# Optimization experiments

Measured on AMD Instinct MI355X. Metric: run time of the kernel, lower is better.

## Reference

```python
import jax, jax.numpy as jnp
import numpy as np
from jax import lax

SPATIAL = 4
PAD = 1
STRIDE = 1


def _route(x, rconv_w, rconv_b, fc_w, fc_b, num_experts):
    # x: (b, c, h, w); adaptive avg pool to (SPATIAL, SPATIAL) -- h,w divisible by SPATIAL
    b, c, h, w = x.shape
    pooled = x.reshape(b, c, SPATIAL, h // SPATIAL, SPATIAL, w // SPATIAL).mean(axis=(3, 5))
    # 1x1 conv: (b,c,s,s) x (rc,c) -> (b,rc,s,s)
    y = jnp.einsum('bcij,rc->brij', pooled, rconv_w) + rconv_b[None, :, None, None]
    y = jax.nn.relu(y).reshape(b, -1)                      # (b, rc*s*s)
    y = jax.nn.relu(y @ fc_w.T + fc_b)                     # (b, num_experts*c)
    y = y.reshape(b, num_experts, c)
    return jax.nn.sigmoid(y)                               # (b, k, c)


def _conv_per_sample(xi, wi):
    # xi: (c_in, h, w), wi: (c_out, c_in, kh, kw)
    out = lax.conv_general_dilated(
        xi[None], wi, window_strides=(STRIDE, STRIDE),
        padding=[(PAD, PAD), (PAD, PAD)],
        dimension_numbers=('NCHW', 'OIHW', 'NCHW'))
    return out[0]


def setup_inputs() -> dict:
    key = jax.random.key(0)
    ks = jax.random.split(key, 6)
    b, c_in, c_out, kk, ne = 16, 256, 256, 3, 3
    rc = max(c_in // 16, 16)  # reduction_channels = 16
    x = jax.random.normal(ks[0], (b, c_in, 64, 64), dtype=jnp.float32)
    expert_weight = jax.random.normal(ks[1], (ne, c_out, c_in, kk, kk), dtype=jnp.float32) * 0.02
    rconv_w = jax.random.normal(ks[2], (rc, c_in), dtype=jnp.float32) * 0.05
    rconv_b = jax.random.normal(ks[3], (rc,), dtype=jnp.float32) * 0.05
    fc_w = jax.random.normal(ks[4], (ne * c_in, rc * SPATIAL * SPATIAL), dtype=jnp.float32) * 0.05
    fc_b = jax.random.normal(ks[5], (ne * c_in,), dtype=jnp.float32) * 0.05
    return {"x": x, "expert_weight": expert_weight, "rconv_w": rconv_w,
            "rconv_b": rconv_b, "fc_w": fc_w, "fc_b": fc_b}


def reference(x, expert_weight, rconv_w, rconv_b, fc_w, fc_b):
    ne = expert_weight.shape[0]
    r = _route(x, rconv_w, rconv_b, fc_w, fc_b, ne)        # (b, k, c_in)
    # per-sample combined weights: routing scales input channels of each expert kernel
    w = jnp.einsum('bkc,kocij->bocij', r, expert_weight)    # (b, c_out, c_in, kh, kw)
    out = jax.vmap(_conv_per_sample)(x, w)                  # (b, c_out, h', w')
    return out
```

## Files before the change

kernel.cpp:

```cpp
#include <hip/hip_runtime.h>

#define B_   16
#define C_   256
#define OC_  256
#define H_   64
#define W_   64
#define NE_  3

typedef __attribute__((ext_vector_type(8))) __bf16 bf16x8;
typedef __attribute__((ext_vector_type(4))) float  f32x4;

__device__ __forceinline__ short f2bf(float f) {
    unsigned u = __float_as_uint(f);
    u += 0x7fffu + ((u >> 16) & 1u);
    return (short)(u >> 16);
}

__device__ __forceinline__ void gll16(const void* g, void* l) {
    __builtin_amdgcn_global_load_lds(
        (const __attribute__((address_space(1))) unsigned int*)g,
        (__attribute__((address_space(3))) unsigned int*)l,
        16, 0, 0);
}

__global__ __launch_bounds__(256) void k_transpose_pool(
        const float* __restrict__ x, short* __restrict__ xt, float* __restrict__ pooled) {
    int y = blockIdx.x;
    int b = blockIdx.y;
    int t = threadIdx.x;
    int si = y >> 4;
    __shared__ float tile[64 * 65];

    for (int cc = 0; cc < 4; ++cc) {
        int cbase = cc * 64;
        for (int q = 0; q < 16; ++q) {
            int c_l = q * 4 + (t >> 6);
            int xx  = t & 63;
            tile[c_l * 65 + xx] =
                x[(((size_t)b * C_ + cbase + c_l) * H_ + y) * W_ + xx];
        }
        __syncthreads();
        {
            int c_l = t & 63, sj = t >> 6;
            float s = 0.f;
            #pragma unroll
            for (int u = 0; u < 16; ++u) s += tile[c_l * 65 + sj * 16 + u];
            atomicAdd(&pooled[((b * 4 + si) * 4 + sj) * 256 + cbase + c_l], s);
        }
        for (int q = 0; q < 16; ++q) {
            int c_l = t & 63;
            int xx  = q * 4 + (t >> 6);
            xt[(((size_t)b * H_ + y) * W_ + xx) * C_ + cbase + c_l] =
                f2bf(tile[c_l * 65 + xx]);
        }
        __syncthreads();
    }
}

__global__ __launch_bounds__(256) void k_route(
        const float* __restrict__ pooled, const float* __restrict__ rconv_w,
        const float* __restrict__ rconv_b, const float* __restrict__ fc_w,
        const float* __restrict__ fc_b, float* __restrict__ r_buf) {
    int b = blockIdx.x;
    int t = threadIdx.x;
    __shared__ float pl[16][257];
    __shared__ float y1[256];

    #pragma unroll
    for (int q = 0; q < 16; ++q)
        pl[q][t] = pooled[b * 4096 + q * 256 + t] * (1.0f / 256.0f);
    __syncthreads();
    {
        int rcc = t >> 4, ss = t & 15;
        float acc = rconv_b[rcc];
        #pragma unroll 8
        for (int c = 0; c < 256; ++c)
            acc += pl[ss][c] * rconv_w[rcc * 256 + c];
        y1[rcc * 16 + ss] = fmaxf(acc, 0.f);
    }
    __syncthreads();
    for (int e0 = 0; e0 < 768; e0 += 256) {
        int e = e0 + t;
        float acc = fc_b[e];
        #pragma unroll 8
        for (int q = 0; q < 256; ++q)
            acc += y1[q] * fc_w[(size_t)e * 256 + q];
        acc = fmaxf(acc, 0.f);
        r_buf[(size_t)b * 768 + e] = 1.f / (1.f + __expf(-acc));
    }
}

__global__ __launch_bounds__(256) void k_combine(
        const float* __restrict__ E, const float* __restrict__ r_buf,
        short* __restrict__ wcomb) {
    int o = blockIdx.x;
    int t = threadIdx.x;
    __shared__ float eT[3][2304];
    #pragma unroll
    for (int k = 0; k < 3; ++k)
        #pragma unroll
        for (int q = 0; q < 9; ++q)
            eT[k][q * 256 + t] = E[((size_t)k * OC_ + o) * 2304 + q * 256 + t];
    __syncthreads();
    int c = t;
    for (int b = 0; b < 16; ++b) {
        float r0 = r_buf[(size_t)b * 768 + c];
        float r1 = r_buf[(size_t)b * 768 + 256 + c];
        float r2 = r_buf[(size_t)b * 768 + 512 + c];
        short* wo = wcomb + ((size_t)(b * OC_ + o) * 9) * C_;
        #pragma unroll
        for (int tap = 0; tap < 9; ++tap) {
            float v = r0 * eT[0][c * 9 + tap] + r1 * eT[1][c * 9 + tap]
                    + r2 * eT[2][c * 9 + tap];
            wo[tap * C_ + c] = f2bf(v);
        }
    }
}

__global__ __launch_bounds__(256) void k_conv(
        const short* __restrict__ xt, const short* __restrict__ wcomb,
        float* __restrict__ out, const short* __restrict__ zbuf) {
    int lin  = blockIdx.x;
    int work = (lin & 7) * 128 + (lin >> 3);
    int b      = work >> 6;
    int o_base = ((work >> 5) & 1) * 128;
    int y0     = (work & 31) * 2;

    int t = threadIdx.x;
    int lane = t & 63, w = t >> 6;
    int quad = lane >> 4, l15 = lane & 15;

    __shared__ __align__(16) short aT[128 * 64];
    __shared__ __align__(16) short bT[128 * 64];

    const short* aBase[4];
    int bRow[4], bXX[4], bCS[4];
    #pragma unroll
    for (int r = 0; r < 4; ++r) {
        int g = r * 256 + t;
        int row = g >> 3, ch8 = g & 7;
        int cs = ch8 ^ (row & 7);
        aBase[r] = wcomb + ((size_t)(b * OC_ + o_base + row)) * 9 * C_ + cs * 8;
        bRow[r] = row >> 6; bXX[r] = row & 63; bCS[r] = cs;
    }

    f32x4 acc[4][4];
    #pragma unroll
    for (int i = 0; i < 4; ++i)
        #pragma unroll
        for (int j = 0; j < 4; ++j) acc[i][j] = {0.f, 0.f, 0.f, 0.f};

    int m_base = (w & 1) * 64;
    int n_base = (w >> 1) * 64;

    for (int tap = 0; tap < 9; ++tap) {
        int ti = tap / 3, tj = tap % 3;
        const short* bBase[4];
        #pragma unroll
        for (int r = 0; r < 4; ++r) {
            int yy = y0 + bRow[r] + ti - 1;
            int xc = bXX[r] + tj - 1;
            bool valid = ((unsigned)yy < (unsigned)H_) && ((unsigned)xc < (unsigned)W_);
            bBase[r] = valid
                ? xt + ((size_t)(b * H_ + yy) * W_ + xc) * C_ + bCS[r] * 8
                : zbuf;
        }
        #pragma unroll
        for (int cc = 0; cc < 4; ++cc) {
            int kc = tap * 4 + cc;
            __syncthreads();
            #pragma unroll
            for (int r = 0; r < 4; ++r)
                gll16(aBase[r] + kc * 64, &aT[((r << 8) + (w << 6)) * 8]);
            #pragma unroll
            for (int r = 0; r < 4; ++r)
                gll16(bBase[r] + cc * 64, &bT[((r << 8) + (w << 6)) * 8]);
            __syncthreads();

            #pragma unroll
            for (int s = 0; s < 2; ++s) {
                int slot = ((s * 4 + quad) ^ (l15 & 7)) * 8;
                bf16x8 af[4], bfv[4];
                #pragma unroll
                for (int mb = 0; mb < 4; ++mb)
                    af[mb] = *(const bf16x8*)&aT[(m_base + mb * 16 + l15) * 64 + slot];
                #pragma unroll
                for (int nb = 0; nb < 4; ++nb)
                    bfv[nb] = *(const bf16x8*)&bT[(n_base + nb * 16 + l15) * 64 + slot];
                #pragma unroll
                for (int mb = 0; mb < 4; ++mb)
                    #pragma unroll
                    for (int nb = 0; nb < 4; ++nb)
                        acc[mb][nb] = __builtin_amdgcn_mfma_f32_16x16x32_bf16(
                            af[mb], bfv[nb], acc[mb][nb], 0, 0, 0);
            }
        }
    }

    #pragma unroll
    for (int mb = 0; mb < 4; ++mb) {
        #pragma unroll
        for (int nb = 0; nb < 4; ++nb) {
            int p  = n_base + nb * 16 + l15;
            int yy = y0 + (p >> 6);
            int xx = p & 63;
            #pragma unroll
            for (int rg = 0; rg < 4; ++rg) {
                int o = o_base + m_base + mb * 16 + quad * 4 + rg;
                out[(((size_t)b * OC_ + o) * H_ + yy) * W_ + xx] = acc[mb][nb][rg];
            }
        }
    }
}

extern "C" void kernel_launch(void* const* d_in, const int* in_sizes, int n_in,
                              void* d_out, int out_size, void* d_ws, size_t ws_size,
                              hipStream_t stream) {
    const float* x       = (const float*)d_in[0];
    const float* E       = (const float*)d_in[1];
    const float* rconv_w = (const float*)d_in[2];
    const float* rconv_b = (const float*)d_in[3];
    const float* fc_w    = (const float*)d_in[4];
    const float* fc_b    = (const float*)d_in[5];
    float* out = (float*)d_out;

    char* ws = (char*)d_ws;
    short* xt     = (short*)(ws);
    short* wcomb  = (short*)(ws + 33554432);
    float* pooled = (float*)(ws + 52428800);
    float* rbuf   = (float*)(ws + 52690944);
    short* zbuf   = (short*)(ws + 52740096);

    hipMemsetAsync(zbuf, 0, 1024, stream);
    hipMemsetAsync(pooled, 0, 262144, stream);

    k_transpose_pool<<<dim3(64, 16), 256, 0, stream>>>(x, xt, pooled);
    k_route<<<dim3(16), 256, 0, stream>>>(pooled, rconv_w, rconv_b, fc_w, fc_b, rbuf);
    k_combine<<<dim3(256), 256, 0, stream>>>(E, rbuf, wcomb);
    k_conv<<<dim3(1024), 256, 0, stream>>>(xt, wcomb, out, zbuf);
}
```

Before: 261.8 us.

## Stage input window once per channel chunk, double-buffer weights, vectorize transpose

```diff
diff --git a/kernel.cpp b/kernel.cpp
--- a/kernel.cpp
+++ b/kernel.cpp
@@ -5,7 +5,6 @@
 #define OC_  256
 #define H_   64
 #define W_   64
-#define NE_  3
 
 typedef __attribute__((ext_vector_type(8))) __bf16 bf16x8;
 typedef __attribute__((ext_vector_type(4))) float  f32x4;
@@ -15,7 +14,9 @@
     u += 0x7fffu + ((u >> 16) & 1u);
     return (short)(u >> 16);
 }
-
+__device__ __forceinline__ unsigned pk2(float a, float b) {
+    return (unsigned(f2bf(a)) & 0xffffu) | (unsigned(f2bf(b)) << 16);
+}
 __device__ __forceinline__ void gll16(const void* g, void* l) {
     __builtin_amdgcn_global_load_lds(
         (const __attribute__((address_space(1))) unsigned int*)g,
@@ -25,35 +26,40 @@
 
 __global__ __launch_bounds__(256) void k_transpose_pool(
         const float* __restrict__ x, short* __restrict__ xt, float* __restrict__ pooled) {
-    int y = blockIdx.x;
-    int b = blockIdx.y;
-    int t = threadIdx.x;
+    int y = blockIdx.x, b = blockIdx.y, t = threadIdx.x;
     int si = y >> 4;
-    __shared__ float tile[64 * 65];
+    int lane = t & 63, wv = t >> 6;
+    int xq = lane & 15, cw = lane >> 4;
+    __shared__ float tile[64 * 67];
 
     for (int cc = 0; cc < 4; ++cc) {
         int cbase = cc * 64;
-        for (int q = 0; q < 16; ++q) {
-            int c_l = q * 4 + (t >> 6);
-            int xx  = t & 63;
-            tile[c_l * 65 + xx] =
-                x[(((size_t)b * C_ + cbase + c_l) * H_ + y) * W_ + xx];
+        if (cc) __syncthreads();
+        #pragma unroll
+        for (int r = 0; r < 4; ++r) {
+            int c_l = r * 16 + wv * 4 + cw;
+            float4 v = *(const float4*)&x[(((size_t)b * C_ + cbase + c_l) * H_ + y) * W_ + xq * 4];
+            float* tp = &tile[c_l * 67 + xq * 4];
+            tp[0] = v.x; tp[1] = v.y; tp[2] = v.z; tp[3] = v.w;
+            float s = v.x + v.y + v.z + v.w;
+            s += __shfl_xor(s, 1);
+            s += __shfl_xor(s, 2);
+            if ((lane & 3) == 0)
+                atomicAdd(&pooled[((b * 4 + si) * 4 + (xq >> 2)) * 256 + cbase + c_l], s);
         }
         __syncthreads();
-        {
-            int c_l = t & 63, sj = t >> 6;
-            float s = 0.f;
+        #pragma unroll
+        for (int r2 = 0; r2 < 2; ++r2) {
+            int u = r2 * 256 + t;
+            int xx = u >> 3, cgl = u & 7;
+            float f[8];
             #pragma unroll
-            for (int u = 0; u < 16; ++u) s += tile[c_l * 65 + sj * 16 + u];
-            atomicAdd(&pooled[((b * 4 + si) * 4 + sj) * 256 + cbase + c_l], s);
-        }
-        for (int q = 0; q < 16; ++q) {
-            int c_l = t & 63;
-            int xx  = q * 4 + (t >> 6);
-            xt[(((size_t)b * H_ + y) * W_ + xx) * C_ + cbase + c_l] =
-                f2bf(tile[c_l * 65 + xx]);
-        }
-        __syncthreads();
+            for (int j = 0; j < 8; ++j) f[j] = tile[(cgl * 8 + j) * 67 + xx];
+            uint4 pkv;
+            pkv.x = pk2(f[0], f[1]); pkv.y = pk2(f[2], f[3]);
+            pkv.z = pk2(f[4], f[5]); pkv.w = pk2(f[6], f[7]);
+            *(uint4*)&xt[(((size_t)b * H_ + y) * W_ + xx) * C_ + cbase + cgl * 8] = pkv;
+        }
     }
 }
 
@@ -94,6 +100,7 @@
         const float* __restrict__ E, const float* __restrict__ r_buf,
         short* __restrict__ wcomb) {
     int o = blockIdx.x;
+    int b0 = blockIdx.y * 4;
     int t = threadIdx.x;
     __shared__ float eT[3][2304];
     #pragma unroll
@@ -103,7 +110,9 @@
             eT[k][q * 256 + t] = E[((size_t)k * OC_ + o) * 2304 + q * 256 + t];
     __syncthreads();
     int c = t;
-    for (int b = 0; b < 16; ++b) {
+    #pragma unroll
+    for (int bb = 0; bb < 4; ++bb) {
+        int b = b0 + bb;
         float r0 = r_buf[(size_t)b * 768 + c];
         float r1 = r_buf[(size_t)b * 768 + 256 + c];
         float r2 = r_buf[(size_t)b * 768 + 512 + c];
@@ -117,7 +126,7 @@
     }
 }
 
-__global__ __launch_bounds__(256) void k_conv(
+__global__ __launch_bounds__(256, 2) void k_conv(
         const short* __restrict__ xt, const short* __restrict__ wcomb,
         float* __restrict__ out, const short* __restrict__ zbuf) {
     int lin  = blockIdx.x;
@@ -130,70 +139,90 @@
     int lane = t & 63, w = t >> 6;
     int quad = lane >> 4, l15 = lane & 15;
 
-    __shared__ __align__(16) short aT[128 * 64];
-    __shared__ __align__(16) short bT[128 * 64];
-
-    const short* aBase[4];
-    int bRow[4], bXX[4], bCS[4];
+    __shared__ __align__(16) short win[4 * 64 * 64];
+    __shared__ __align__(16) short abuf[2][128 * 64];
+
+    const short* wsrc[8];
+    #pragma unroll
+    for (int r = 0; r < 8; ++r) {
+        int u = r * 256 + t;
+        int pos = u >> 3, sp = u & 7;
+        int wrow = pos >> 6, xc = pos & 63;
+        int yy = y0 - 1 + wrow;
+        int ss = sp ^ (xc & 7);
+        wsrc[r] = ((unsigned)yy < 64u)
+            ? xt + (((size_t)b * 64 + yy) * 64 + xc) * 256 + ss * 8
+            : zbuf;
+    }
+    const short* asrc[4];
     #pragma unroll
     for (int r = 0; r < 4; ++r) {
-        int g = r * 256 + t;
-        int row = g >> 3, ch8 = g & 7;
-        int cs = ch8 ^ (row & 7);
-        aBase[r] = wcomb + ((size_t)(b * OC_ + o_base + row)) * 9 * C_ + cs * 8;
-        bRow[r] = row >> 6; bXX[r] = row & 63; bCS[r] = cs;
-    }
-
-    f32x4 acc[4][4];
-    #pragma unroll
-    for (int i = 0; i < 4; ++i)
-        #pragma unroll
-        for (int j = 0; j < 4; ++j) acc[i][j] = {0.f, 0.f, 0.f, 0.f};
+        int u = r * 256 + t;
+        int o_l = u >> 3, sp = u & 7;
+        int ss = sp ^ (o_l & 7);
+        asrc[r] = wcomb + (((size_t)b * 256 + o_base + o_l) * 9) * 256 + ss * 8;
+    }
 
     int m_base = (w & 1) * 64;
     int n_base = (w >> 1) * 64;
-
-    for (int tap = 0; tap < 9; ++tap) {
-        int ti = tap / 3, tj = tap % 3;
-        const short* bBase[4];
-        #pragma unroll
-        for (int r = 0; r < 4; ++r) {
-            int yy = y0 + bRow[r] + ti - 1;
-            int xc = bXX[r] + tj - 1;
-            bool valid = ((unsigned)yy < (unsigned)H_) && ((unsigned)xc < (unsigned)W_);
-            bBase[r] = valid
-                ? xt + ((size_t)(b * H_ + yy) * W_ + xc) * C_ + bCS[r] * 8
-                : zbuf;
-        }
-        #pragma unroll
-        for (int cc = 0; cc < 4; ++cc) {
-            int kc = tap * 4 + cc;
-            __syncthreads();
-            #pragma unroll
-            for (int r = 0; r < 4; ++r)
-                gll16(aBase[r] + kc * 64, &aT[((r << 8) + (w << 6)) * 8]);
-            #pragma unroll
-            for (int r = 0; r < 4; ++r)
-                gll16(bBase[r] + cc * 64, &bT[((r << 8) + (w << 6)) * 8]);
-            __syncthreads();
-
+    int ry0 = n_base >> 6;
+    int xb[4];
+    #pragma unroll
+    for (int nb = 0; nb < 4; ++nb) xb[nb] = nb * 16 + l15;
+
+    f32x4 acc[4][4];
+    #pragma unroll
+    for (int i = 0; i < 4; ++i)
+        #pragma unroll
+        for (int j = 0; j < 4; ++j) acc[i][j] = {0.f, 0.f, 0.f, 0.f};
+
+    for (int cc = 0; cc < 4; ++cc) {
+        int ccOff = cc * 64;
+        #pragma unroll
+        for (int r = 0; r < 8; ++r)
+            gll16(wsrc[r] + ccOff, &win[(r * 256 + w * 64) * 8]);
+        #pragma unroll
+        for (int r = 0; r < 4; ++r)
+            gll16(asrc[r] + ccOff, &abuf[0][(r * 256 + w * 64) * 8]);
+        __syncthreads();
+
+        #pragma unroll
+        for (int tap = 0; tap < 9; ++tap) {
+            const int ti = tap / 3, tj = tap % 3;
+            const int cur = tap & 1;
+            if (tap < 8) {
+                int off2 = (tap + 1) * 256 + ccOff;
+                #pragma unroll
+                for (int r = 0; r < 4; ++r)
+                    gll16(asrc[r] + off2, &abuf[cur ^ 1][(r * 256 + w * 64) * 8]);
+            }
+            int wrb = (ry0 + ti) * 4096;
             #pragma unroll
             for (int s = 0; s < 2; ++s) {
-                int slot = ((s * 4 + quad) ^ (l15 & 7)) * 8;
-                bf16x8 af[4], bfv[4];
-                #pragma unroll
-                for (int mb = 0; mb < 4; ++mb)
-                    af[mb] = *(const bf16x8*)&aT[(m_base + mb * 16 + l15) * 64 + slot];
-                #pragma unroll
-                for (int nb = 0; nb < 4; ++nb)
-                    bfv[nb] = *(const bf16x8*)&bT[(n_base + nb * 16 + l15) * 64 + slot];
+                int slog = s * 4 + quad;
+                bf16x8 af[4], bv[4];
+                #pragma unroll
+                for (int mb = 0; mb < 4; ++mb) {
+                    int o_l = m_base + mb * 16 + l15;
+                    af[mb] = *(const bf16x8*)&abuf[cur][o_l * 64 + ((slog ^ (o_l & 7)) * 8)];
+                }
+                #pragma unroll
+                for (int nb = 0; nb < 4; ++nb) {
+                    int xc = xb[nb] + (tj - 1);
+                    bool ok = ((unsigned)xc < 64u);
+                    int xs = ok ? xc : 0;
+                    bf16x8 v = *(const bf16x8*)&win[wrb + xs * 64 + ((slog ^ (xs & 7)) * 8)];
+                    bf16x8 zz = {};
+                    bv[nb] = ok ? v : zz;
+                }
                 #pragma unroll
                 for (int mb = 0; mb < 4; ++mb)
                     #pragma unroll
                     for (int nb = 0; nb < 4; ++nb)
                         acc[mb][nb] = __builtin_amdgcn_mfma_f32_16x16x32_bf16(
-                            af[mb], bfv[nb], acc[mb][nb], 0, 0, 0);
+                            af[mb], bv[nb], acc[mb][nb], 0, 0, 0);
             }
+            __syncthreads();
         }
     }
 
@@ -228,14 +257,13 @@
     short* xt     = (short*)(ws);
     short* wcomb  = (short*)(ws + 33554432);
     float* pooled = (float*)(ws + 52428800);
-    float* rbuf   = (float*)(ws + 52690944);
-    short* zbuf   = (short*)(ws + 52740096);
-
-    hipMemsetAsync(zbuf, 0, 1024, stream);
-    hipMemsetAsync(pooled, 0, 262144, stream);
+    short* zbuf   = (short*)(ws + 52690944);
+    float* rbuf   = (float*)(ws + 52692992);
+
+    hipMemsetAsync(pooled, 0, 262144 + 1024, stream);
 
     k_transpose_pool<<<dim3(64, 16), 256, 0, stream>>>(x, xt, pooled);
     k_route<<<dim3(16), 256, 0, stream>>>(pooled, rconv_w, rconv_b, fc_w, fc_b, rbuf);
-    k_combine<<<dim3(256), 256, 0, stream>>>(E, rbuf, wcomb);
+    k_combine<<<dim3(256, 4), 256, 0, stream>>>(E, rbuf, wcomb);
     k_conv<<<dim3(1024), 256, 0, stream>>>(xt, wcomb, out, zbuf);
 }
```

After: 243.9 us. 6.9% less time.
